# Kernel tuning notes

Hardware: AMD Instinct MI355X
Metric: run time of the kernel (lower is better)

## Reference

```python
import jax, jax.numpy as jnp
import numpy as np

B, T, D, H = 64, 512, 1024, 2048


def setup_inputs() -> dict:
    key = jax.random.key(0)
    ks = jax.random.split(key, 7)
    s_ih = 1.0 / np.sqrt(H)
    return {
        "x": jax.random.normal(ks[0], (B, T, D), dtype=jnp.float32),
        "W_ih": jax.random.normal(ks[1], (4 * H, D), dtype=jnp.float32) * s_ih,
        "W_hh": jax.random.normal(ks[2], (4 * H, H), dtype=jnp.float32) * s_ih,
        "b_ih": jax.random.normal(ks[3], (4 * H,), dtype=jnp.float32) * s_ih,
        "b_hh": jax.random.normal(ks[4], (4 * H,), dtype=jnp.float32) * s_ih,
        "W_head": jax.random.normal(ks[5], (D, H), dtype=jnp.float32) * (1.0 / np.sqrt(H)),
        "b_head": jax.random.normal(ks[6], (D,), dtype=jnp.float32) * 0.01,
    }


def reference(x, W_ih, W_hh, b_ih, b_hh, W_head, b_head):
    Bn, Tn, Dn = x.shape
    Hn = W_hh.shape[1]
    # precompute input projections for all timesteps: [T, B, 4H]
    x_proj = jnp.einsum('btd,gd->tbg', x, W_ih) + (b_ih + b_hh)

    def step(carry, xp_t):
        h, c = carry
        gates = xp_t + h @ W_hh.T  # [B, 4H]
        i, f, g, o = jnp.split(gates, 4, axis=-1)  # PyTorch gate order: i,f,g,o
        i = jax.nn.sigmoid(i)
        f = jax.nn.sigmoid(f)
        g = jnp.tanh(g)
        o = jax.nn.sigmoid(o)
        c = f * c + i * g
        h = o * jnp.tanh(c)
        return (h, c), None

    h0 = jnp.zeros((Bn, Hn), dtype=x.dtype)
    c0 = jnp.zeros((Bn, Hn), dtype=x.dtype)
    (h, c), _ = jax.lax.scan(step, (h0, c0), x_proj)
    return h @ W_head.T + b_head  # [B, D]
```

## Files before the change

### kernel.cpp

```cpp
#include <hip/hip_runtime.h>
#include <hip/hip_bf16.h>
#include <cstdint>
#include <cstddef>

#define BB 64
#define TT 512
#define DD 1024
#define HH 2048
#define GG 8192

typedef unsigned short u16;
typedef __attribute__((ext_vector_type(8))) short bf16x8;
typedef __attribute__((ext_vector_type(4))) float f32x4;

__device__ __forceinline__ u16 f2bf(float f) {
  union { float f; uint32_t u; } v; v.f = f;
  uint32_t r = v.u + 0x7FFFu + ((v.u >> 16) & 1u);
  return (u16)(r >> 16);
}
__device__ __forceinline__ float bf2f(u16 h) {
  union { uint32_t u; float f; } v; v.u = ((uint32_t)h) << 16; return v.f;
}

__device__ __forceinline__ bf16x8 cvt8(const float* __restrict__ p) {
  float4 a = *(const float4*)p;
  float4 b = *(const float4*)(p + 4);
  bf16x8 r;
  r[0] = (short)f2bf(a.x); r[1] = (short)f2bf(a.y);
  r[2] = (short)f2bf(a.z); r[3] = (short)f2bf(a.w);
  r[4] = (short)f2bf(b.x); r[5] = (short)f2bf(b.y);
  r[6] = (short)f2bf(b.z); r[7] = (short)f2bf(b.w);
  return r;
}

__device__ __forceinline__ bf16x8 cohload16(const u16* p) {
  bf16x8 v;
  asm volatile("global_load_dwordx4 %0, %1, off sc0 sc1" : "=v"(v) : "v"(p));
  return v;
}
__device__ __forceinline__ void cohstore16(u16* p, bf16x8 v) {
  asm volatile("global_store_dwordx4 %0, %1, off sc0 sc1" :: "v"(p), "v"(v) : "memory");
}
__device__ __forceinline__ int get_xcd() {
  int x;
  asm("s_getreg_b32 %0, hwreg(20, 0, 32)" : "=s"(x));
  return x & 7;
}

__global__ void conv_wih_kernel(const float* __restrict__ W, u16* __restrict__ Wb) {
  size_t idx = (size_t)blockIdx.x * blockDim.x + threadIdx.x;
  if (idx >= (size_t)GG * DD / 8) return;
  *(bf16x8*)(Wb + idx * 8) = cvt8(W + idx * 8);
}

__global__ void conv_xT_kernel(const float* __restrict__ x, u16* __restrict__ xbT) {
  size_t idx = (size_t)blockIdx.x * blockDim.x + threadIdx.x;
  if (idx >= (size_t)BB * TT * DD / 8) return;
  const int col8 = (int)(idx & 127);
  const int row = (int)(idx >> 7);
  const int b = row >> 9, t = row & 511;
  bf16x8 v = cvt8(x + (size_t)row * DD + col8 * 8);
  *(bf16x8*)(xbT + ((size_t)t * BB + b) * DD + col8 * 8) = v;
}

template<int XMODE>
__global__ __launch_bounds__(512, 1)
void lstm_persistent(const float* __restrict__ x, const u16* __restrict__ xbT,
                     const u16* __restrict__ wihb, const float* __restrict__ W_hh,
                     const float* __restrict__ b_ih, const float* __restrict__ b_hh,
                     u16* __restrict__ h0, u16* __restrict__ h1,
                     int* __restrict__ arrv, int* __restrict__ gof,
                     int* __restrict__ ximp, int* __restrict__ xcdcnt,
                     u16* __restrict__ staged) {
  __shared__ u16 Wlds[64 * 2 * 64 * 8];
  __shared__ float red[4 * 2 * 64 * 4];
  __shared__ float gst[64 * 36];
  __shared__ u16 hsh[512];
  __shared__ int sxcd, srank;

  const int tid = threadIdx.x;
  const int wave = tid >> 6, lane = tid & 63;
  const int m = wave & 3, khalf = wave >> 2;
  const int c = lane & 15, g = lane >> 4;
  const int wg = blockIdx.x, j0 = wg * 8;

  if (tid == 0) {
    const int xd = get_xcd();
    sxcd = xd;
    srank = __hip_atomic_fetch_add(xcdcnt + xd * 16, 1, __ATOMIC_RELAXED,
                                   __HIP_MEMORY_SCOPE_AGENT);
  }

  {
    const int r = tid >> 4;
    const int gr = (r < 8) ? (j0 + r) : (r < 16) ? (HH + j0 + r - 8)
                 : (r < 24) ? (2 * HH + j0 + r - 16) : (3 * HH + j0 + r - 24);
    const int which = r >> 4, cc = r & 15;
    const float* src = W_hh + (size_t)gr * HH;
    const int k0 = (tid & 15) * 128;
    #pragma unroll
    for (int k8 = 0; k8 < 16; ++k8) {
      const int k = k0 + k8 * 8;
      bf16x8 v = cvt8(src + k);
      const int ent = ((k >> 5) * 2 + which) * 64 + ((k >> 3) & 3) * 16 + cc;
      *(bf16x8*)(Wlds + (size_t)ent * 8) = v;
    }
  }

  const int tb = tid >> 3, tj = tid & 7;
  const int jg = j0 + tj;
  const float bia = b_ih[jg] + b_hh[jg];
  const float bfa = b_ih[HH + jg] + b_hh[HH + jg];
  const float bga = b_ih[2 * HH + jg] + b_hh[2 * HH + jg];
  const float boa = b_ih[3 * HH + jg] + b_hh[3 * HH + jg];
  float cst = 0.f;

  const int arow = m * 16 + c;
  const int r0 = (c < 8) ? (j0 + c) : (HH + j0 + c - 8);
  const int r1 = (c < 8) ? (2 * HH + j0 + c) : (3 * HH + j0 + c - 8);

  __syncthreads();
  const int xcd = sxcd, rank = srank & 31;
  int* xctr = ximp + xcd * 16;

  for (int t = 0; t < TT; ++t) {
    const u16* hs = (t & 1) ? h1 : h0;
    u16* hd = (t & 1) ? h0 : h1;
    u16* stg = staged + ((size_t)xcd * 2 + (t & 1)) * ((size_t)BB * HH);
    f32x4 acc0 = {0.f, 0.f, 0.f, 0.f};
    f32x4 acc1 = {0.f, 0.f, 0.f, 0.f};

    #pragma unroll 4
    for (int i = 0; i < 16; ++i) {
      const int k = khalf * 512 + i * 32 + g * 8;
      bf16x8 a;
      if constexpr (XMODE == 1) a = *(const bf16x8*)(xbT + ((size_t)t * BB + arow) * DD + k);
      else                      a = cvt8(x + ((size_t)arow * TT + t) * DD + k);
      bf16x8 b0 = *(const bf16x8*)(wihb + (size_t)r0 * DD + k);
      bf16x8 b1 = *(const bf16x8*)(wihb + (size_t)r1 * DD + k);
      acc0 = __builtin_amdgcn_mfma_f32_16x16x32_bf16(a, b0, acc0, 0, 0, 0);
      acc1 = __builtin_amdgcn_mfma_f32_16x16x32_bf16(a, b1, acc1, 0, 0, 0);
    }

    if (t > 0) {
      if (wg == 0) {
        if (tid < 256) {
          int iters = 0;
          while (__hip_atomic_load(arrv + tid * 16, __ATOMIC_RELAXED, __HIP_MEMORY_SCOPE_AGENT) < t) {
            __builtin_amdgcn_s_sleep(1);
            if (++iters > (1 << 17)) break;
          }
        }
        __syncthreads();
        if (tid < 256)
          __hip_atomic_store(gof + tid * 16, t, __ATOMIC_RELAXED, __HIP_MEMORY_SCOPE_AGENT);
      } else {
        if (tid == 0) {
          int iters = 0;
          while (__hip_atomic_load(gof + wg * 16, __ATOMIC_RELAXED, __HIP_MEMORY_SCOPE_AGENT) < t) {
            __builtin_amdgcn_s_sleep(1);
            if (++iters > (1 << 17)) break;
          }
        }
      }
    }
    __syncthreads();

    {
      const int row = rank * 2 + (tid >> 8);
      const int col = (tid & 255) * 8;
      bf16x8 v = cohload16(hs + (size_t)row * HH + col);
      asm volatile("s_waitcnt vmcnt(0)" ::: "memory");
      *(bf16x8*)(stg + (size_t)row * HH + col) = v;
    }
    __syncthreads();
    if (tid == 0) {
      __hip_atomic_fetch_add(xctr, 1, __ATOMIC_RELAXED, __HIP_MEMORY_SCOPE_AGENT);
      int iters = 0;
      while (__hip_atomic_load(xctr, __ATOMIC_RELAXED, __HIP_MEMORY_SCOPE_AGENT) < 32 * (t + 1)) {
        __builtin_amdgcn_s_sleep(1);
        if (++iters > (1 << 17)) break;
      }
      asm volatile("buffer_inv sc0" ::: "memory");
      asm volatile("s_waitcnt vmcnt(0)" ::: "memory");
    }
    __syncthreads();

    {
      bf16x8 hf[32];
      const u16* hrow = stg + (size_t)arow * HH + g * 8;
      #pragma unroll
      for (int i = 0; i < 32; ++i)
        hf[i] = *(const bf16x8*)(hrow + (size_t)(khalf * 32 + i) * 32);
      #pragma unroll
      for (int i = 0; i < 32; ++i) {
        const int kb = khalf * 32 + i;
        bf16x8 b0 = *(const bf16x8*)(Wlds + (size_t)((kb * 2 + 0) * 64 + lane) * 8);
        bf16x8 b1 = *(const bf16x8*)(Wlds + (size_t)((kb * 2 + 1) * 64 + lane) * 8);
        acc0 = __builtin_amdgcn_mfma_f32_16x16x32_bf16(hf[i], b0, acc0, 0, 0, 0);
        acc1 = __builtin_amdgcn_mfma_f32_16x16x32_bf16(hf[i], b1, acc1, 0, 0, 0);
      }
    }

    if (khalf == 1) {
      #pragma unroll
      for (int q = 0; q < 4; ++q) {
        red[((m * 2 + 0) * 64 + lane) * 4 + q] = acc0[q];
        red[((m * 2 + 1) * 64 + lane) * 4 + q] = acc1[q];
      }
    }
    __syncthreads();
    if (khalf == 0) {
      #pragma unroll
      for (int q = 0; q < 4; ++q) {
        const float s0 = acc0[q] + red[((m * 2 + 0) * 64 + lane) * 4 + q];
        const float s1 = acc1[q] + red[((m * 2 + 1) * 64 + lane) * 4 + q];
        const int b = m * 16 + g * 4 + q;
        gst[b * 36 + c] = s0;
        gst[b * 36 + 16 + c] = s1;
      }
    }
    __syncthreads();

    {
      const float ip = gst[tb * 36 + tj]      + bia;
      const float fp = gst[tb * 36 + 8 + tj]  + bfa;
      const float gp = gst[tb * 36 + 16 + tj] + bga;
      const float op = gst[tb * 36 + 24 + tj] + boa;
      const float ig = 1.f / (1.f + expf(-ip));
      const float fg = 1.f / (1.f + expf(-fp));
      const float gv = tanhf(gp);
      const float og = 1.f / (1.f + expf(-op));
      cst = fg * cst + ig * gv;
      hsh[tb * 8 + tj] = f2bf(og * tanhf(cst));
    }
    __syncthreads();

    if (tid < 64) {
      bf16x8 v = *(const bf16x8*)(hsh + tid * 8);
      cohstore16(hd + (size_t)tid * HH + j0, v);
      asm volatile("s_waitcnt vmcnt(0)" ::: "memory");
    }
    if (tid == 0)
      __hip_atomic_store(arrv + wg * 16, t + 1, __ATOMIC_RELAXED, __HIP_MEMORY_SCOPE_AGENT);
  }
}

__global__ __launch_bounds__(512)
void lstm_step_kernel(const float* __restrict__ x,
                      const float* __restrict__ W_ih, const float* __restrict__ W_hh,
                      const float* __restrict__ b_ih, const float* __restrict__ b_hh,
                      const u16* __restrict__ h_src, u16* __restrict__ h_dst,
                      float* __restrict__ cbuf, int t) {
  const int tid = threadIdx.x;
  const int wave = tid >> 6, lane = tid & 63;
  const int m = wave & 3, khalf = wave >> 2;
  const int j0 = blockIdx.x * 8;
  const int c = lane & 15;
  const int arow = m * 16 + c;
  const int koff = (lane >> 4) * 8;
  const int r0 = (c < 8) ? (j0 + c) : (HH + j0 + c - 8);
  const int r1 = (c < 8) ? (2 * HH + j0 + c) : (3 * HH + j0 + c - 8);

  f32x4 acc0 = {0.f, 0.f, 0.f, 0.f};
  f32x4 acc1 = {0.f, 0.f, 0.f, 0.f};

  if (khalf == 0) {
    const size_t xrow = ((size_t)arow * TT + t) * DD;
    #pragma unroll 4
    for (int kb = 0; kb < 32; ++kb) {
      const int k = kb * 32 + koff;
      bf16x8 a = cvt8(x + xrow + k);
      bf16x8 b0 = cvt8(W_ih + (size_t)r0 * DD + k);
      bf16x8 b1 = cvt8(W_ih + (size_t)r1 * DD + k);
      acc0 = __builtin_amdgcn_mfma_f32_16x16x32_bf16(a, b0, acc0, 0, 0, 0);
      acc1 = __builtin_amdgcn_mfma_f32_16x16x32_bf16(a, b1, acc1, 0, 0, 0);
    }
    #pragma unroll 4
    for (int kb = 0; kb < 16; ++kb) {
      const int kh = kb * 32 + koff;
      bf16x8 a = *(const bf16x8*)(h_src + (size_t)arow * HH + kh);
      bf16x8 b0 = cvt8(W_hh + (size_t)r0 * HH + kh);
      bf16x8 b1 = cvt8(W_hh + (size_t)r1 * HH + kh);
      acc0 = __builtin_amdgcn_mfma_f32_16x16x32_bf16(a, b0, acc0, 0, 0, 0);
      acc1 = __builtin_amdgcn_mfma_f32_16x16x32_bf16(a, b1, acc1, 0, 0, 0);
    }
  } else {
    #pragma unroll 4
    for (int kb = 0; kb < 48; ++kb) {
      const int kh = 512 + kb * 32 + koff;
      bf16x8 a = *(const bf16x8*)(h_src + (size_t)arow * HH + kh);
      bf16x8 b0 = cvt8(W_hh + (size_t)r0 * HH + kh);
      bf16x8 b1 = cvt8(W_hh + (size_t)r1 * HH + kh);
      acc0 = __builtin_amdgcn_mfma_f32_16x16x32_bf16(a, b0, acc0, 0, 0, 0);
      acc1 = __builtin_amdgcn_mfma_f32_16x16x32_bf16(a, b1, acc1, 0, 0, 0);
    }
  }

  __shared__ float red[4][2][64][4];
  if (khalf == 1) {
    #pragma unroll
    for (int q = 0; q < 4; ++q) { red[m][0][lane][q] = acc0[q]; red[m][1][lane][q] = acc1[q]; }
  }
  __syncthreads();
  if (khalf == 1) return;
  #pragma unroll
  for (int q = 0; q < 4; ++q) { acc0[q] += red[m][0][lane][q]; acc1[q] += red[m][1][lane][q]; }

  const float bias0 = b_ih[r0] + b_hh[r0];
  const float bias1 = b_ih[r1] + b_hh[r1];
  #pragma unroll
  for (int q = 0; q < 4; ++q) { acc0[q] += bias0; acc1[q] += bias1; }

  float fpre[4], opre[4];
  #pragma unroll
  for (int q = 0; q < 4; ++q) {
    fpre[q] = __shfl_xor(acc0[q], 8);
    opre[q] = __shfl_xor(acc1[q], 8);
  }

  if (c < 8) {
    const int j = j0 + c;
    #pragma unroll
    for (int q = 0; q < 4; ++q) {
      const int b = m * 16 + (lane >> 4) * 4 + q;
      const float ig = 1.f / (1.f + expf(-acc0[q]));
      const float fg = 1.f / (1.f + expf(-fpre[q]));
      const float gg = tanhf(acc1[q]);
      const float og = 1.f / (1.f + expf(-opre[q]));
      const float cold = cbuf[(size_t)b * HH + j];
      const float cn = fg * cold + ig * gg;
      cbuf[(size_t)b * HH + j] = cn;
      h_dst[(size_t)b * HH + j] = f2bf(og * tanhf(cn));
    }
  }
}

__global__ __launch_bounds__(256)
void head_kernel(const u16* __restrict__ hfin, const float* __restrict__ W_head,
                 const float* __restrict__ b_head, float* __restrict__ out) {
  const int tid = threadIdx.x, wave = tid >> 6, lane = tid & 63;
  const int m = wave;
  const int c = lane & 15;
  const int koff = (lane >> 4) * 8;
  const int d = blockIdx.x * 16 + c;
  const int arow = m * 16 + c;
  f32x4 acc = {0.f, 0.f, 0.f, 0.f};
  #pragma unroll 4
  for (int kb = 0; kb < 64; ++kb) {
    const int k = kb * 32 + koff;
    bf16x8 a = *(const bf16x8*)(hfin + (size_t)arow * HH + k);
    bf16x8 b = cvt8(W_head + (size_t)d * HH + k);
    acc = __builtin_amdgcn_mfma_f32_16x16x32_bf16(a, b, acc, 0, 0, 0);
  }
  const float bh = b_head[d];
  #pragma unroll
  for (int q = 0; q < 4; ++q) {
    const int b = m * 16 + (lane >> 4) * 4 + q;
    out[(size_t)b * DD + d] = acc[q] + bh;
  }
}

extern "C" void kernel_launch(void* const* d_in, const int* in_sizes, int n_in,
                              void* d_out, int out_size, void* d_ws, size_t ws_size,
                              hipStream_t stream) {
  const float* x      = (const float*)d_in[0];
  const float* W_ih   = (const float*)d_in[1];
  const float* W_hh   = (const float*)d_in[2];
  const float* b_ih   = (const float*)d_in[3];
  const float* b_hh   = (const float*)d_in[4];
  const float* W_head = (const float*)d_in[5];
  const float* b_head = (const float*)d_in[6];
  float* out = (float*)d_out;

  char* ws = (char*)d_ws;
  u16*  h0     = (u16*)(ws + 0);
  u16*  h1     = (u16*)(ws + 256 * 1024);
  int*  arrv   = (int*)(ws + 512 * 1024);
  int*  gof    = (int*)(ws + 544 * 1024);
  int*  ximp   = (int*)(ws + 576 * 1024);
  int*  xcdcnt = (int*)(ws + 608 * 1024);
  float* cbuf  = (float*)(ws + 512 * 1024);
  u16*  staged = (u16*)(ws + (1ull << 20));
  u16*  wihb   = (u16*)(ws + (5ull << 20));
  u16*  xbT    = (u16*)(ws + (21ull << 20));

  const size_t NEED1 = (85ull << 20);
  const size_t NEED0 = (21ull << 20);

  hipMemsetAsync(ws, 0, 1u << 20, stream);

  if (ws_size >= NEED0) {
    {
      const int n8 = (int)((size_t)GG * DD / 8);
      conv_wih_kernel<<<(n8 + 255) / 256, 256, 0, stream>>>(W_ih, wihb);
    }
    if (ws_size >= NEED1) {
      const int n8 = (int)((size_t)BB * TT * DD / 8);
      conv_xT_kernel<<<(n8 + 255) / 256, 256, 0, stream>>>(x, xbT);
      lstm_persistent<1><<<256, 512, 0, stream>>>(x, xbT, wihb, W_hh, b_ih, b_hh,
                                                  h0, h1, arrv, gof, ximp, xcdcnt, staged);
    } else {
      lstm_persistent<0><<<256, 512, 0, stream>>>(x, xbT, wihb, W_hh, b_ih, b_hh,
                                                  h0, h1, arrv, gof, ximp, xcdcnt, staged);
    }
  } else {
    for (int t = 0; t < TT; ++t) {
      u16* hs = (t & 1) ? h1 : h0;
      u16* hd = (t & 1) ? h0 : h1;
      lstm_step_kernel<<<256, 512, 0, stream>>>(x, W_ih, W_hh, b_ih, b_hh, hs, hd, cbuf, t);
    }
  }

  head_kernel<<<64, 256, 0, stream>>>(h0, W_head, b_head, out);
}
```

Baseline: 11.76 ms.

## Replace centralized grid barrier with per-wave point-to-point producer/consumer flags

Drops the two-level barrier (block 0 gathering arrivals then releasing everyone, plus a per-XCD counter) in the persistent LSTM recurrence. Each wave now polls only the producer flags for the h slice it imports into the XCD-local staging buffer, publishes a per-wave import flag, and then polls only the import flags for the rows it consumes. This removes the serialized hop through block 0 and several __syncthreads per timestep. The h output buffer is double-buffered in LDS, and the workspace memset is enlarged to cover the staging area. In exchange there is more flag polling traffic, and correctness depends on the new index mapping matching producers to consumers exactly.

New measurement: 11.23 ms. 1.05x faster.

```diff
diff --git a/kernel.cpp b/kernel.cpp
--- a/kernel.cpp
+++ b/kernel.cpp
@@ -17,9 +17,6 @@
   union { float f; uint32_t u; } v; v.f = f;
   uint32_t r = v.u + 0x7FFFu + ((v.u >> 16) & 1u);
   return (u16)(r >> 16);
-}
-__device__ __forceinline__ float bf2f(u16 h) {
-  union { uint32_t u; float f; } v; v.u = ((uint32_t)h) << 16; return v.f;
 }
 
 __device__ __forceinline__ bf16x8 cvt8(const float* __restrict__ p) {
@@ -69,19 +66,18 @@
                      const u16* __restrict__ wihb, const float* __restrict__ W_hh,
                      const float* __restrict__ b_ih, const float* __restrict__ b_hh,
                      u16* __restrict__ h0, u16* __restrict__ h1,
-                     int* __restrict__ arrv, int* __restrict__ gof,
-                     int* __restrict__ ximp, int* __restrict__ xcdcnt,
-                     u16* __restrict__ staged) {
+                     int* __restrict__ pflag, int* __restrict__ iflag,
+                     int* __restrict__ xcdcnt, u16* __restrict__ staged) {
   __shared__ u16 Wlds[64 * 2 * 64 * 8];
   __shared__ float red[4 * 2 * 64 * 4];
   __shared__ float gst[64 * 36];
-  __shared__ u16 hsh[512];
+  __shared__ u16 hsh[2][512];
   __shared__ int sxcd, srank;
 
   const int tid = threadIdx.x;
   const int wave = tid >> 6, lane = tid & 63;
   const int m = wave & 3, khalf = wave >> 2;
-  const int c = lane & 15, g = lane >> 4;
+  const int c = lane & 15, lofs = lane >> 4;
   const int wg = blockIdx.x, j0 = wg * 8;
 
   if (tid == 0) {
@@ -121,7 +117,14 @@
 
   __syncthreads();
   const int xcd = sxcd, rank = srank & 31;
-  int* xctr = ximp + xcd * 16;
+  const int g_imp = rank >> 2, q_imp = rank & 3;
+  const int imp_row = q_imp * 16 + 2 * wave + (lane >> 5);
+  const int imp_col = g_imp * 256 + (lane & 31) * 8;
+  const int pf_idx = (g_imp * 32 + (lane & 31)) * 16;
+  const int cons_gi = (lane >> 3) & 3, cons_w = lane & 7;
+  const int cons_rank = (4 * khalf + cons_gi) * 4 + m;
+  const int if_idx = ((xcd * 32 + cons_rank) * 8 + cons_w) * 16;
+  const int my_if_idx = ((xcd * 32 + rank) * 8 + wave) * 16;
 
   for (int t = 0; t < TT; ++t) {
     const u16* hs = (t & 1) ? h1 : h0;
@@ -132,7 +135,7 @@
 
     #pragma unroll 4
     for (int i = 0; i < 16; ++i) {
-      const int k = khalf * 512 + i * 32 + g * 8;
+      const int k = khalf * 512 + i * 32 + lofs * 8;
       bf16x8 a;
       if constexpr (XMODE == 1) a = *(const bf16x8*)(xbT + ((size_t)t * BB + arow) * DD + k);
       else                      a = cvt8(x + ((size_t)arow * TT + t) * DD + k);
@@ -143,52 +146,42 @@
     }
 
     if (t > 0) {
-      if (wg == 0) {
-        if (tid < 256) {
-          int iters = 0;
-          while (__hip_atomic_load(arrv + tid * 16, __ATOMIC_RELAXED, __HIP_MEMORY_SCOPE_AGENT) < t) {
-            __builtin_amdgcn_s_sleep(1);
-            if (++iters > (1 << 17)) break;
-          }
+      {
+        int iters = 0;
+        while (true) {
+          int v = __hip_atomic_load(pflag + pf_idx, __ATOMIC_RELAXED, __HIP_MEMORY_SCOPE_AGENT);
+          if (__all(v >= t)) break;
+          __builtin_amdgcn_s_sleep(1);
+          if (++iters > (1 << 17)) break;
         }
-        __syncthreads();
-        if (tid < 256)
-          __hip_atomic_store(gof + tid * 16, t, __ATOMIC_RELAXED, __HIP_MEMORY_SCOPE_AGENT);
-      } else {
-        if (tid == 0) {
-          int iters = 0;
-          while (__hip_atomic_load(gof + wg * 16, __ATOMIC_RELAXED, __HIP_MEMORY_SCOPE_AGENT) < t) {
-            __builtin_amdgcn_s_sleep(1);
-            if (++iters > (1 << 17)) break;
-          }
+        asm volatile("" ::: "memory");
+        __builtin_amdgcn_sched_barrier(0);
+        bf16x8 v = cohload16(hs + (size_t)imp_row * HH + imp_col);
+        asm volatile("s_waitcnt vmcnt(0)" ::: "memory");
+        *(bf16x8*)(stg + (size_t)imp_row * HH + imp_col) = v;
+        asm volatile("s_waitcnt vmcnt(0)" ::: "memory");
+        if (lane == 0)
+          __hip_atomic_store(iflag + my_if_idx, t, __ATOMIC_RELAXED, __HIP_MEMORY_SCOPE_AGENT);
+      }
+      {
+        int iters = 0;
+        while (true) {
+          int v = __hip_atomic_load(iflag + if_idx, __ATOMIC_RELAXED, __HIP_MEMORY_SCOPE_AGENT);
+          if (__all(v >= t)) break;
+          __builtin_amdgcn_s_sleep(1);
+          if (++iters > (1 << 17)) break;
         }
+        asm volatile("" ::: "memory");
+        __builtin_amdgcn_sched_barrier(0);
       }
     }
-    __syncthreads();
-
-    {
-      const int row = rank * 2 + (tid >> 8);
-      const int col = (tid & 255) * 8;
-      bf16x8 v = cohload16(hs + (size_t)row * HH + col);
-      asm volatile("s_waitcnt vmcnt(0)" ::: "memory");
-      *(bf16x8*)(stg + (size_t)row * HH + col) = v;
-    }
-    __syncthreads();
-    if (tid == 0) {
-      __hip_atomic_fetch_add(xctr, 1, __ATOMIC_RELAXED, __HIP_MEMORY_SCOPE_AGENT);
-      int iters = 0;
-      while (__hip_atomic_load(xctr, __ATOMIC_RELAXED, __HIP_MEMORY_SCOPE_AGENT) < 32 * (t + 1)) {
-        __builtin_amdgcn_s_sleep(1);
-        if (++iters > (1 << 17)) break;
-      }
-      asm volatile("buffer_inv sc0" ::: "memory");
-      asm volatile("s_waitcnt vmcnt(0)" ::: "memory");
-    }
-    __syncthreads();
+    asm volatile("buffer_inv sc0" ::: "memory");
+    asm volatile("s_waitcnt vmcnt(0)" ::: "memory");
+    __builtin_amdgcn_sched_barrier(0);
 
     {
       bf16x8 hf[32];
-      const u16* hrow = stg + (size_t)arow * HH + g * 8;
+      const u16* hrow = stg + (size_t)arow * HH + lofs * 8;
       #pragma unroll
       for (int i = 0; i < 32; ++i)
         hf[i] = *(const bf16x8*)(hrow + (size_t)(khalf * 32 + i) * 32);
@@ -215,7 +208,7 @@
       for (int q = 0; q < 4; ++q) {
         const float s0 = acc0[q] + red[((m * 2 + 0) * 64 + lane) * 4 + q];
         const float s1 = acc1[q] + red[((m * 2 + 1) * 64 + lane) * 4 + q];
-        const int b = m * 16 + g * 4 + q;
+        const int b = m * 16 + lofs * 4 + q;
         gst[b * 36 + c] = s0;
         gst[b * 36 + 16 + c] = s1;
       }
@@ -232,17 +225,17 @@
       const float gv = tanhf(gp);
       const float og = 1.f / (1.f + expf(-op));
       cst = fg * cst + ig * gv;
-      hsh[tb * 8 + tj] = f2bf(og * tanhf(cst));
+      hsh[t & 1][tb * 8 + tj] = f2bf(og * tanhf(cst));
     }
     __syncthreads();
 
     if (tid < 64) {
-      bf16x8 v = *(const bf16x8*)(hsh + tid * 8);
+      bf16x8 v = *(const bf16x8*)(&hsh[t & 1][tid * 8]);
       cohstore16(hd + (size_t)tid * HH + j0, v);
       asm volatile("s_waitcnt vmcnt(0)" ::: "memory");
     }
     if (tid == 0)
-      __hip_atomic_store(arrv + wg * 16, t + 1, __ATOMIC_RELAXED, __HIP_MEMORY_SCOPE_AGENT);
+      __hip_atomic_store(pflag + wg * 16, t + 1, __ATOMIC_RELAXED, __HIP_MEMORY_SCOPE_AGENT);
   }
 }
 
@@ -376,10 +369,9 @@
   char* ws = (char*)d_ws;
   u16*  h0     = (u16*)(ws + 0);
   u16*  h1     = (u16*)(ws + 256 * 1024);
-  int*  arrv   = (int*)(ws + 512 * 1024);
-  int*  gof    = (int*)(ws + 544 * 1024);
-  int*  ximp   = (int*)(ws + 576 * 1024);
-  int*  xcdcnt = (int*)(ws + 608 * 1024);
+  int*  pflag  = (int*)(ws + 512 * 1024);
+  int*  iflag  = (int*)(ws + 544 * 1024);
+  int*  xcdcnt = (int*)(ws + 672 * 1024);
   float* cbuf  = (float*)(ws + 512 * 1024);
   u16*  staged = (u16*)(ws + (1ull << 20));
   u16*  wihb   = (u16*)(ws + (5ull << 20));
@@ -388,7 +380,7 @@
   const size_t NEED1 = (85ull << 20);
   const size_t NEED0 = (21ull << 20);
 
-  hipMemsetAsync(ws, 0, 1u << 20, stream);
+  hipMemsetAsync(ws, 0, 5u << 20, stream);
 
   if (ws_size >= NEED0) {
     {
@@ -399,10 +391,10 @@
       const int n8 = (int)((size_t)BB * TT * DD / 8);
       conv_xT_kernel<<<(n8 + 255) / 256, 256, 0, stream>>>(x, xbT);
       lstm_persistent<1><<<256, 512, 0, stream>>>(x, xbT, wihb, W_hh, b_ih, b_hh,
-                                                  h0, h1, arrv, gof, ximp, xcdcnt, staged);
+                                                  h0, h1, pflag, iflag, xcdcnt, staged);
     } else {
       lstm_persistent<0><<<256, 512, 0, stream>>>(x, xbT, wihb, W_hh, b_ih, b_hh,
-                                                  h0, h1, arrv, gof, ximp, xcdcnt, staged);
+                                                  h0, h1, pflag, iflag, xcdcnt, staged);
     }
   } else {
     for (int t = 0; t < TT; ++t) {
```
